# Performance work log

Hardware: AMD Instinct MI355X
Metric: run time of the kernel (lower is better)

The kernel has to match this reference:

```python
import jax, jax.numpy as jnp
import numpy as np
import math

V, D, H, L, T, B = 50257, 1024, 16, 8, 1024, 4
HD = D // H
EPS = 1e-5


def setup_inputs() -> dict:
    key = jax.random.key(0)
    ks = jax.random.split(key, 8)
    s = 0.02
    inp = {
        'context': jax.random.randint(ks[0], (B, T), 0, V, dtype=jnp.int32),
        'targets': jax.random.randint(ks[1], (B, T), 0, V, dtype=jnp.int32),
        'wte': jax.random.normal(ks[2], (V, D), jnp.float32) * s,  # tied with lm_head
        'wpe': jax.random.normal(ks[3], (T, D), jnp.float32) * s,
        'ln1_g': jnp.ones((L, D), jnp.float32), 'ln1_b': jnp.zeros((L, D), jnp.float32),
        'w_attn': jax.random.normal(ks[4], (L, 3 * D, D), jnp.float32) * s,
        'w_proj': jax.random.normal(ks[5], (L, D, D), jnp.float32) * s,
        'ln2_g': jnp.ones((L, D), jnp.float32), 'ln2_b': jnp.zeros((L, D), jnp.float32),
        'w_fc': jax.random.normal(ks[6], (L, 4 * D, D), jnp.float32) * s,
        'w_out': jax.random.normal(ks[7], (L, D, 4 * D), jnp.float32) * s,
        'lnf_g': jnp.ones((D,), jnp.float32), 'lnf_b': jnp.zeros((D,), jnp.float32),
    }
    return inp


def layer_norm(x, g, b):
    mu = jnp.mean(x, axis=-1, keepdims=True)
    var = jnp.var(x, axis=-1, keepdims=True)
    return (x - mu) * jax.lax.rsqrt(var + EPS) * g + b


def attention(x, w_attn, w_proj):
    # x: [B,T,D]; w_attn: [3D,D] (torch Linear convention: y = x @ W^T)
    qkv = x @ w_attn.T  # [B,T,3D]
    q, k, v = jnp.split(qkv, 3, axis=-1)
    q = q.reshape(B, T, H, HD).transpose(0, 2, 1, 3)  # [B,H,T,hd]
    k = k.reshape(B, T, H, HD).transpose(0, 2, 1, 3)
    v = v.reshape(B, T, H, HD).transpose(0, 2, 1, 3)
    att = jnp.einsum('bhtd,bhsd->bhts', q, k) * (1.0 / math.sqrt(HD))
    causal = jnp.tril(jnp.ones((T, T), dtype=bool))
    att = jnp.where(causal, att, -jnp.inf)
    att = jax.nn.softmax(att, axis=-1)
    y = jnp.einsum('bhts,bhsd->bhtd', att, v)
    y = y.transpose(0, 2, 1, 3).reshape(B, T, D)
    return y @ w_proj.T


def mlp(x, w_fc, w_out):
    h = jax.nn.gelu(x @ w_fc.T, approximate=False)  # exact GELU = torch nn.GELU()
    return h @ w_out.T


def reference(context, targets, wte, wpe, ln1_g, ln1_b, w_attn, w_proj,
              ln2_g, ln2_b, w_fc, w_out, lnf_g, lnf_b):
    x = wte[context] + wpe[jnp.arange(T)]  # [B,T,D]
    for i in range(L):
        x = x + attention(layer_norm(x, ln1_g[i], ln1_b[i]), w_attn[i], w_proj[i])
        x = x + mlp(layer_norm(x, ln2_g[i], ln2_b[i]), w_fc[i], w_out[i])
    x = layer_norm(x, lnf_g, lnf_b)
    logits = x @ wte.T  # tied lm_head, [B,T,V]
    # cross entropy with ignore_index=-1
    logp = jax.nn.log_softmax(logits, axis=-1)
    tgt = targets.reshape(-1)
    valid = tgt != -1
    safe_tgt = jnp.where(valid, tgt, 0)
    nll = -jnp.take_along_axis(logp.reshape(-1, V), safe_tgt[:, None], axis=-1)[:, 0]
    loss = jnp.sum(jnp.where(valid, nll, 0.0)) / jnp.maximum(jnp.sum(valid), 1)
    return logits, loss
```

## Files before the change

kernel.cpp:

```cpp
#include <hip/hip_runtime.h>
#include <cstdint>

#define V_SIZE 50257
#define V_PAD  50432
#define D_DIM  1024
#define H_NUM  16
#define L_NUM  8
#define T_LEN  1024
#define B_NUM  4
#define HD_DIM 64
#define M_ROWS 4096
#define LN_EPS 1e-5f

typedef __attribute__((ext_vector_type(8))) __bf16 bf16x8;
typedef __attribute__((ext_vector_type(4))) float f32x4;
typedef __attribute__((ext_vector_type(8))) unsigned short u16x8;

__device__ __forceinline__ unsigned short f2bf(float f) {
  unsigned u = __builtin_bit_cast(unsigned, f);
  u += 0x7fffu + ((u >> 16) & 1u);
  return (unsigned short)(u >> 16);
}

__device__ __forceinline__ void gload_lds16(const void* g, void* l) {
  typedef const __attribute__((address_space(1))) unsigned int* gp_t;
  typedef __attribute__((address_space(3))) unsigned int* lp_t;
  __builtin_amdgcn_global_load_lds((gp_t)g, (lp_t)l, 16, 0, 0);
}

#define BARSB() { __builtin_amdgcn_s_barrier(); __builtin_amdgcn_sched_barrier(0); }
#define LGKM0() { asm volatile("s_waitcnt lgkmcnt(0)" ::: "memory"); __builtin_amdgcn_sched_barrier(0); }

__global__ __launch_bounds__(256) void embed_kernel(const int* __restrict__ ctx,
                                                    const float* __restrict__ wte,
                                                    const float* __restrict__ wpe,
                                                    float* __restrict__ x) {
  int i = blockIdx.x * blockDim.x + threadIdx.x;
  if (i >= M_ROWS * D_DIM) return;
  int bt = i / D_DIM, d = i - bt * D_DIM;
  int t = bt & (T_LEN - 1);
  x[i] = wte[(size_t)ctx[bt] * D_DIM + d] + wpe[(size_t)t * D_DIM + d];
}

__global__ __launch_bounds__(256) void conv_layer_kernel(const float* __restrict__ wa,
                                                         const float* __restrict__ wp,
                                                         const float* __restrict__ wf,
                                                         const float* __restrict__ wo,
                                                         unsigned short* __restrict__ oa,
                                                         unsigned short* __restrict__ op,
                                                         unsigned short* __restrict__ of,
                                                         unsigned short* __restrict__ oo) {
  long i = (long)(blockIdx.x * 256 + threadIdx.x) * 8;
  const float* src; unsigned short* dst; long off;
  if (i < 3145728L)      { src = wa; dst = oa; off = i; }
  else if (i < 4194304L) { src = wp; dst = op; off = i - 3145728L; }
  else if (i < 8388608L) { src = wf; dst = of; off = i - 4194304L; }
  else                   { src = wo; dst = oo; off = i - 8388608L; }
  float4 v0 = *(const float4*)(src + off);
  float4 v1 = *(const float4*)(src + off + 4);
  u16x8 o;
  o[0] = f2bf(v0.x); o[1] = f2bf(v0.y); o[2] = f2bf(v0.z); o[3] = f2bf(v0.w);
  o[4] = f2bf(v1.x); o[5] = f2bf(v1.y); o[6] = f2bf(v1.z); o[7] = f2bf(v1.w);
  *(u16x8*)(dst + off) = o;
}

__global__ __launch_bounds__(256) void conv_kernel(const float* __restrict__ in,
                                                   unsigned short* __restrict__ out, long n) {
  long i = (long)(blockIdx.x * 256 + threadIdx.x) * 8;
  if (i >= n) return;
  float4 v0 = *(const float4*)(in + i);
  float4 v1 = *(const float4*)(in + i + 4);
  u16x8 o;
  o[0] = f2bf(v0.x); o[1] = f2bf(v0.y); o[2] = f2bf(v0.z); o[3] = f2bf(v0.w);
  o[4] = f2bf(v1.x); o[5] = f2bf(v1.y); o[6] = f2bf(v1.z); o[7] = f2bf(v1.w);
  *(u16x8*)(out + i) = o;
}

__global__ __launch_bounds__(256) void layernorm_kernel(const float* __restrict__ x,
                                                        const float* __restrict__ g,
                                                        const float* __restrict__ b,
                                                        unsigned short* __restrict__ o) {
  int r = blockIdx.x;
  int tid = threadIdx.x;
  const float* row = x + (size_t)r * D_DIM;
  float4 v = *(const float4*)(row + tid * 4);
  float s  = v.x + v.y + v.z + v.w;
  float s2 = v.x * v.x + v.y * v.y + v.z * v.z + v.w * v.w;
  #pragma unroll
  for (int off = 32; off; off >>= 1) {
    s  += __shfl_xor(s, off);
    s2 += __shfl_xor(s2, off);
  }
  __shared__ float a1[4], a2[4];
  int w = tid >> 6, lane = tid & 63;
  if (lane == 0) { a1[w] = s; a2[w] = s2; }
  __syncthreads();
  s  = a1[0] + a1[1] + a1[2] + a1[3];
  s2 = a2[0] + a2[1] + a2[2] + a2[3];
  float mu  = s * (1.0f / D_DIM);
  float var = s2 * (1.0f / D_DIM) - mu * mu;
  float rs  = rsqrtf(var + LN_EPS);
  int d = tid * 4;
  float4 gv = *(const float4*)(g + d);
  float4 bv = *(const float4*)(b + d);
  ushort4 ov;
  ov.x = f2bf((v.x - mu) * rs * gv.x + bv.x);
  ov.y = f2bf((v.y - mu) * rs * gv.y + bv.y);
  ov.z = f2bf((v.z - mu) * rs * gv.z + bv.z);
  ov.w = f2bf((v.w - mu) * rs * gv.w + bv.w);
  *(ushort4*)(o + (size_t)r * D_DIM + d) = ov;
}

template<int EPI>
__global__ __launch_bounds__(256) void mfma_gemm(const unsigned short* __restrict__ A,
                                                 const unsigned short* __restrict__ W,
                                                 const float* R, void* Cout,
                                                 int K, int ldc, int nreal) {
  __shared__ unsigned short As[128 * 32];
  __shared__ unsigned short Bs[128 * 32];
  const int tid  = threadIdx.x;
  const int wave = tid >> 6, lane = tid & 63;
  const int wr = wave >> 1, wc = wave & 1;
  const long row0 = (long)blockIdx.y * 128;
  const long col0 = (long)blockIdx.x * 128;
  f32x4 acc[4][4] = {};
  const int frow = lane & 15;
  const int fk   = (lane >> 4) * 8;
  const int b0 = wave * 2048 + lane * 16;
  for (int k0 = 0; k0 < K; k0 += 32) {
    #pragma unroll
    for (int c = 0; c < 2; ++c) {
      int b = b0 + c * 1024;
      int r = b >> 6, ke = (b & 63) >> 1;
      gload_lds16(A + (row0 + r) * (long)K + k0 + ke, (char*)As + b);
      gload_lds16(W + (col0 + r) * (long)K + k0 + ke, (char*)Bs + b);
    }
    __syncthreads();
    bf16x8 af[4], bfr[4];
    #pragma unroll
    for (int i = 0; i < 4; ++i)
      af[i] = *(const bf16x8*)(As + (wr * 64 + i * 16 + frow) * 32 + fk);
    #pragma unroll
    for (int j = 0; j < 4; ++j)
      bfr[j] = *(const bf16x8*)(Bs + (wc * 64 + j * 16 + frow) * 32 + fk);
    #pragma unroll
    for (int i = 0; i < 4; ++i)
      #pragma unroll
      for (int j = 0; j < 4; ++j)
        acc[i][j] = __builtin_amdgcn_mfma_f32_16x16x32_bf16(af[i], bfr[j], acc[i][j], 0, 0, 0);
    __syncthreads();
  }
  const int crow = (lane >> 4) * 4;
  const int ccol = lane & 15;
  #pragma unroll
  for (int i = 0; i < 4; ++i) {
    #pragma unroll
    for (int r = 0; r < 4; ++r) {
      long row = row0 + wr * 64 + i * 16 + crow + r;
      #pragma unroll
      for (int j = 0; j < 4; ++j) {
        long col = col0 + wc * 64 + j * 16 + ccol;
        float v = acc[i][j][r];
        if (EPI == 1) {
          ((float*)Cout)[row * (long)ldc + col] = v + R[row * (long)ldc + col];
        } else {
          ((float*)Cout)[row * (long)ldc + col] = v;
        }
      }
    }
  }
}

__device__ __forceinline__ void stage_chunk8(const unsigned short* __restrict__ base,
                                             long rbase, int K, long gk,
                                             char* cb, int tid) {
  #pragma unroll
  for (int j = 0; j < 2; ++j) {
    int db = j * 8192 + tid * 16;
    int lb = db ^ (((db >> 7) & 3) << 4);
    long r = lb >> 6;
    int e = (lb & 63) >> 1;
    gload_lds16(base + (rbase + r) * (long)K + gk + e, cb + db);
  }
}

__device__ __forceinline__ bf16x8 rdfrag(const char* cb, int rr, int lhi) {
  int p = (rr << 6) + (lhi << 4);
  p ^= ((rr >> 1) & 3) << 4;
  return *(const bf16x8*)(cb + p);
}

template<int EPI>
__global__ __launch_bounds__(512, 1) void gemm8p(const unsigned short* __restrict__ A,
                                                 const unsigned short* __restrict__ W,
                                                 void* Cout, int K, int ldc, int nreal,
                                                 int nbx, int xcd) {
  __shared__ char lds[131072];
  const int tid  = threadIdx.x;
  const int lane = tid & 63;
  const int wave = tid >> 6;
  const int wr = wave >> 2, wc = wave & 3;
  const int lhi = lane >> 4, llo = lane & 15;
  int bid = blockIdx.x;
  if (xcd) { int per = (int)gridDim.x >> 3; bid = (bid & 7) * per + (bid >> 3); }
  const int brow = bid % nbx;
  const int bcol = bid / nbx;
  const long row0 = (long)brow * 256;
  const long col0 = (long)bcol * 256;
  char* Ab0 = (char*)lds;
  char* Bb0 = (char*)lds + 65536;
  const int nt = K >> 6;

  stage_chunk8(A, row0, K, 0,  Ab0,         tid);
  stage_chunk8(W, col0, K, 0,  Bb0,         tid);
  stage_chunk8(A, row0, K, 32, Ab0 + 16384, tid);
  stage_chunk8(W, col0, K, 32, Bb0 + 16384, tid);
  if (nt > 1) {
    stage_chunk8(A, row0, K, 64, Ab0 + 32768, tid);
    stage_chunk8(W, col0, K, 64, Bb0 + 32768, tid);
    asm volatile("s_waitcnt vmcnt(4)" ::: "memory");
  } else {
    asm volatile("s_waitcnt vmcnt(0)" ::: "memory");
  }
  BARSB();

  f32x4 acc[8][4] = {};
  bf16x8 bb[4];
  for (int t = 0; t < nt; ++t) {
    char* Ac = Ab0 + (t & 1) * 32768;
    char* Bc = Bb0 + (t & 1) * 32768;
    char* An = Ab0 + ((t + 1) & 1) * 32768;
    char* Bn = Bb0 + ((t + 1) & 1) * 32768;
    bf16x8 aa[4];
    #pragma unroll
    for (int m = 0; m < 4; ++m) aa[m] = rdfrag(Ac, wr * 128 + m * 16 + llo, lhi);
    #pragma unroll
    for (int n = 0; n < 4; ++n) bb[n] = rdfrag(Bc, wc * 64 + n * 16 + llo, lhi);
    if (t + 1 < nt) stage_chunk8(A, row0, K, (long)(t + 1) * 64 + 32, An + 16384, tid);
    BARSB(); LGKM0();
    __builtin_amdgcn_s_setprio(1);
    #pragma unroll
    for (int m = 0; m < 4; ++m)
      #pragma unroll
      for (int n = 0; n < 4; ++n)
        acc[m][n] = __builtin_amdgcn_mfma_f32_16x16x32_bf16(aa[m], bb[n], acc[m][n], 0, 0, 0);
    __builtin_amdgcn_s_setprio(0);
    BARSB();
    #pragma unroll
    for (int m = 0; m < 4; ++m) aa[m] = rdfrag(Ac, wr * 128 + 64 + m * 16 + llo, lhi);
    if (t + 1 < nt) stage_chunk8(W, col0, K, (long)(t + 1) * 64 + 32, Bn + 16384, tid);
    BARSB(); LGKM0();
    __builtin_amdgcn_s_setprio(1);
    #pragma unroll
    for (int m = 0; m < 4; ++m)
      #pragma unroll
      for (int n = 0; n < 4; ++n)
        acc[m + 4][n] = __builtin_amdgcn_mfma_f32_16x16x32_bf16(aa[m], bb[n], acc[m + 4][n], 0, 0, 0);
    __builtin_amdgcn_s_setprio(0);
    BARSB();
    #pragma unroll
    for (int m = 0; m < 4; ++m) aa[m] = rdfrag(Ac + 16384, wr * 128 + m * 16 + llo, lhi);
    #pragma unroll
    for (int n = 0; n < 4; ++n) bb[n] = rdfrag(Bc + 16384, wc * 64 + n * 16 + llo, lhi);
    if (t + 2 < nt) stage_chunk8(A, row0, K, (long)(t + 2) * 64, Ac, tid);
    BARSB(); LGKM0();
    __builtin_amdgcn_s_setprio(1);
    #pragma unroll
    for (int m = 0; m < 4; ++m)
      #pragma unroll
      for (int n = 0; n < 4; ++n)
        acc[m][n] = __builtin_amdgcn_mfma_f32_16x16x32_bf16(aa[m], bb[n], acc[m][n], 0, 0, 0);
    __builtin_amdgcn_s_setprio(0);
    BARSB();
    #pragma unroll
    for (int m = 0; m < 4; ++m) aa[m] = rdfrag(Ac + 16384, wr * 128 + 64 + m * 16 + llo, lhi);
    if (t + 2 < nt) stage_chunk8(W, col0, K, (long)(t + 2) * 64, Bc, tid);
    BARSB(); LGKM0();
    __builtin_amdgcn_s_setprio(1);
    #pragma unroll
    for (int m = 0; m < 4; ++m)
      #pragma unroll
      for (int n = 0; n < 4; ++n)
        acc[m + 4][n] = __builtin_amdgcn_mfma_f32_16x16x32_bf16(aa[m], bb[n], acc[m + 4][n], 0, 0, 0);
    __builtin_amdgcn_s_setprio(0);
    if (t < nt - 2) {
      asm volatile("s_waitcnt vmcnt(4)" ::: "memory");
    } else {
      asm volatile("s_waitcnt vmcnt(0)" ::: "memory");
    }
    BARSB();
  }

  #pragma unroll
  for (int mi = 0; mi < 8; ++mi) {
    #pragma unroll
    for (int rg = 0; rg < 4; ++rg) {
      long row = row0 + wr * 128 + mi * 16 + lhi * 4 + rg;
      #pragma unroll
      for (int n = 0; n < 4; ++n) {
        long col = col0 + wc * 64 + n * 16 + llo;
        float v = acc[mi][n][rg];
        if (EPI == 0) {
          if (col < nreal) ((float*)Cout)[row * (long)ldc + col] = v;
        } else if (EPI == 2) {
          float gl = 0.5f * v * (1.0f + erff(v * 0.70710678118654752440f));
          ((unsigned short*)Cout)[row * (long)ldc + col] = f2bf(gl);
        } else {
          ((unsigned short*)Cout)[row * (long)ldc + col] = f2bf(v);
        }
      }
    }
  }
}

__global__ __launch_bounds__(256) void flash_attn_kernel(const unsigned short* __restrict__ qkv,
                                                         unsigned short* __restrict__ y) {
  __shared__ unsigned short Kls[64 * 64];
  __shared__ unsigned short Vtls[64 * 64];
  __shared__ unsigned short Pls[4][16 * 64];
  const int tid = threadIdx.x, wave = tid >> 6, lane = tid & 63;
  const int qt = blockIdx.x;
  const int h = blockIdx.y & (H_NUM - 1), b = blockIdx.y >> 4;
  const int q0 = qt * 64;
  const int lhi = lane >> 4, llo = lane & 15;

  const int qrow = q0 + wave * 16 + llo;
  const unsigned short* qptr =
      qkv + ((size_t)(b * T_LEN + qrow)) * 3072 + h * HD_DIM + lhi * 8;
  const bf16x8 qa0 = *(const bf16x8*)qptr;
  const bf16x8 qa1 = *(const bf16x8*)(qptr + 32);

  f32x4 o[4] = {};
  float m[4] = {-1e30f, -1e30f, -1e30f, -1e30f};
  float l[4] = {0.f, 0.f, 0.f, 0.f};

  const unsigned short* kg = qkv + (size_t)b * T_LEN * 3072 + D_DIM + h * HD_DIM;
  const unsigned short* vg = kg + D_DIM;

  const int krow = tid >> 2, kcol = (tid & 3) * 16;
  const int vs0 = (tid >> 3) * 2, vd0 = (tid & 7) * 8;

  const int ntiles = qt + 1;
  for (int st = 0; st < ntiles; ++st) {
    const int s0 = st * 64;
    {
      const unsigned short* src = kg + (size_t)(s0 + krow) * 3072 + kcol;
      u16x8 a = *(const u16x8*)src;
      u16x8 c = *(const u16x8*)(src + 8);
      int base = krow * 128 + kcol * 2;
      int sw = (krow & 7) << 4;
      *(u16x8*)((char*)Kls + ((base) ^ sw))      = a;
      *(u16x8*)((char*)Kls + ((base + 16) ^ sw)) = c;
    }
    {
      const unsigned short* src = vg + (size_t)(s0 + vs0) * 3072 + vd0;
      u16x8 a = *(const u16x8*)src;
      u16x8 c = *(const u16x8*)(src + 3072);
      #pragma unroll
      for (int j = 0; j < 8; ++j) {
        int d = vd0 + j;
        unsigned val = (unsigned)a[j] | ((unsigned)c[j] << 16);
        *(unsigned*)((char*)Vtls + ((d * 128 + vs0 * 2) ^ ((d & 7) << 4))) = val;
      }
    }
    __syncthreads();

    f32x4 s_acc[4] = {};
    #pragma unroll
    for (int kt = 0; kt < 4; ++kt) {
      int kr = kt * 16 + llo;
      int sw = (kr & 7) << 4;
      bf16x8 kb0 = *(const bf16x8*)((char*)Kls + ((kr * 128 + lhi * 16) ^ sw));
      bf16x8 kb1 = *(const bf16x8*)((char*)Kls + ((kr * 128 + 64 + lhi * 16) ^ sw));
      s_acc[kt] = __builtin_amdgcn_mfma_f32_16x16x32_bf16(qa0, kb0, s_acc[kt], 0, 0, 0);
      s_acc[kt] = __builtin_amdgcn_mfma_f32_16x16x32_bf16(qa1, kb1, s_acc[kt], 0, 0, 0);
    }

    float p[4][4];
    float tmax[4] = {-1e30f, -1e30f, -1e30f, -1e30f};
    const int qg = q0 + wave * 16 + lhi * 4;
    #pragma unroll
    for (int kt = 0; kt < 4; ++kt) {
      int ks = s0 + kt * 16 + llo;
      #pragma unroll
      for (int r = 0; r < 4; ++r) {
        float sv = (ks <= qg + r) ? s_acc[kt][r] * 0.125f : -1e30f;
        p[kt][r] = sv;
        tmax[r] = fmaxf(tmax[r], sv);
      }
    }
    #pragma unroll
    for (int r = 0; r < 4; ++r) {
      #pragma unroll
      for (int off = 1; off < 16; off <<= 1)
        tmax[r] = fmaxf(tmax[r], __shfl_xor(tmax[r], off));
      float mn = fmaxf(m[r], tmax[r]);
      float corr = __expf(m[r] - mn);
      m[r] = mn;
      float ps = 0.f;
      #pragma unroll
      for (int kt = 0; kt < 4; ++kt) {
        p[kt][r] = __expf(p[kt][r] - mn);
        ps += p[kt][r];
      }
      #pragma unroll
      for (int off = 1; off < 16; off <<= 1)
        ps += __shfl_xor(ps, off);
      l[r] = l[r] * corr + ps;
      #pragma unroll
      for (int dt = 0; dt < 4; ++dt) o[dt][r] *= corr;
    }

    unsigned short* pw = Pls[wave];
    #pragma unroll
    for (int r = 0; r < 4; ++r) {
      int q = lhi * 4 + r;
      int sw = (q & 7) << 4;
      #pragma unroll
      for (int kt = 0; kt < 4; ++kt) {
        int k = kt * 16 + llo;
        *(unsigned short*)((char*)pw + ((q * 128 + k * 2) ^ sw)) = f2bf(p[kt][r]);
      }
    }
    asm volatile("s_waitcnt lgkmcnt(0)" ::: "memory");

    int psw = (llo & 7) << 4;
    bf16x8 pa0 = *(const bf16x8*)((char*)pw + ((llo * 128 + lhi * 16) ^ psw));
    bf16x8 pa1 = *(const bf16x8*)((char*)pw + ((llo * 128 + 64 + lhi * 16) ^ psw));
    #pragma unroll
    for (int dt = 0; dt < 4; ++dt) {
      int vr = dt * 16 + llo;
      int sw = (vr & 7) << 4;
      bf16x8 vb0 = *(const bf16x8*)((char*)Vtls + ((vr * 128 + lhi * 16) ^ sw));
      bf16x8 vb1 = *(const bf16x8*)((char*)Vtls + ((vr * 128 + 64 + lhi * 16) ^ sw));
      o[dt] = __builtin_amdgcn_mfma_f32_16x16x32_bf16(pa0, vb0, o[dt], 0, 0, 0);
      o[dt] = __builtin_amdgcn_mfma_f32_16x16x32_bf16(pa1, vb1, o[dt], 0, 0, 0);
    }
    __syncthreads();
  }

  #pragma unroll
  for (int r = 0; r < 4; ++r) {
    long row = q0 + wave * 16 + lhi * 4 + r;
    float inv = 1.0f / l[r];
    #pragma unroll
    for (int dt = 0; dt < 4; ++dt) {
      long col = h * HD_DIM + dt * 16 + llo;
      y[(row + (size_t)b * T_LEN) * D_DIM + col] = f2bf(o[dt][r] * inv);
    }
  }
}

__global__ __launch_bounds__(256) void loss_rows_kernel(const float* __restrict__ logits,
                                                        const int* __restrict__ tgt,
                                                        float* __restrict__ nll,
                                                        float* __restrict__ vld) {
  int r = blockIdx.x;
  int tid = threadIdx.x;
  const float* row = logits + (size_t)r * V_SIZE;
  float mx = -1e30f;
  for (int i = tid; i < V_SIZE; i += 256) mx = fmaxf(mx, row[i]);
  #pragma unroll
  for (int off = 32; off; off >>= 1) mx = fmaxf(mx, __shfl_xor(mx, off));
  __shared__ float sm[4], ss[4];
  int w = tid >> 6, lane = tid & 63;
  if (lane == 0) sm[w] = mx;
  __syncthreads();
  mx = fmaxf(fmaxf(sm[0], sm[1]), fmaxf(sm[2], sm[3]));
  float se = 0.f;
  for (int i = tid; i < V_SIZE; i += 256) se += expf(row[i] - mx);
  #pragma unroll
  for (int off = 32; off; off >>= 1) se += __shfl_xor(se, off);
  if (lane == 0) ss[w] = se;
  __syncthreads();
  if (tid == 0) {
    se = ss[0] + ss[1] + ss[2] + ss[3];
    int tg = tgt[r];
    if (tg != -1) { nll[r] = mx + logf(se) - row[tg]; vld[r] = 1.0f; }
    else          { nll[r] = 0.f;                     vld[r] = 0.f; }
  }
}

__global__ __launch_bounds__(256) void loss_reduce_kernel(const float* __restrict__ nll,
                                                          const float* __restrict__ vld,
                                                          float* __restrict__ out) {
  int tid = threadIdx.x;
  float s = 0.f, c = 0.f;
  for (int i = tid; i < M_ROWS; i += 256) { s += nll[i]; c += vld[i]; }
  #pragma unroll
  for (int off = 32; off; off >>= 1) { s += __shfl_xor(s, off); c += __shfl_xor(c, off); }
  __shared__ float s1[4], s2[4];
  int w = tid >> 6, lane = tid & 63;
  if (lane == 0) { s1[w] = s; s2[w] = c; }
  __syncthreads();
  if (tid == 0) {
    s = s1[0] + s1[1] + s1[2] + s1[3];
    c = s2[0] + s2[1] + s2[2] + s2[3];
    out[0] = s / fmaxf(c, 1.0f);
  }
}

extern "C" void kernel_launch(void* const* d_in, const int* in_sizes, int n_in,
                              void* d_out, int out_size, void* d_ws, size_t ws_size,
                              hipStream_t stream) {
  const int*   ctx    = (const int*)d_in[0];
  const int*   tgt    = (const int*)d_in[1];
  const float* wte    = (const float*)d_in[2];
  const float* wpe    = (const float*)d_in[3];
  const float* ln1_g  = (const float*)d_in[4];
  const float* ln1_b  = (const float*)d_in[5];
  const float* w_attn = (const float*)d_in[6];
  const float* w_proj = (const float*)d_in[7];
  const float* ln2_g  = (const float*)d_in[8];
  const float* ln2_b  = (const float*)d_in[9];
  const float* w_fc   = (const float*)d_in[10];
  const float* w_out  = (const float*)d_in[11];
  const float* lnf_g  = (const float*)d_in[12];
  const float* lnf_b  = (const float*)d_in[13];

  float* outp   = (float*)d_out;
  float* logits = outp;
  float* loss   = outp + (size_t)M_ROWS * V_SIZE;

  char* ws = (char*)d_ws;
  float*          x      = (float*)(ws + 0);
  unsigned short* xn     = (unsigned short*)(ws + 16777216);
  unsigned short* qkv    = (unsigned short*)(ws + 25165824);
  unsigned short* y      = (unsigned short*)(ws + 50331648);
  unsigned short* h      = (unsigned short*)(ws + 58720256);
  unsigned short* wa_bf  = (unsigned short*)(ws + 92274688);
  unsigned short* wp_bf  = (unsigned short*)(ws + 98566144);
  unsigned short* wf_bf  = (unsigned short*)(ws + 100663296);
  unsigned short* wo_bf  = (unsigned short*)(ws + 109051904);
  unsigned short* wte_bf = (unsigned short*)(ws + 25165824);
  float*          nll    = (float*)(ws + 128450560);
  float*          vld    = (float*)(ws + 128466944);

  embed_kernel<<<(M_ROWS * D_DIM + 255) / 256, 256, 0, stream>>>(ctx, wte, wpe, x);

  for (int l = 0; l < L_NUM; ++l) {
    conv_layer_kernel<<<6144, 256, 0, stream>>>(
        w_attn + (size_t)l * 3 * D_DIM * D_DIM, w_proj + (size_t)l * D_DIM * D_DIM,
        w_fc + (size_t)l * 4 * D_DIM * D_DIM, w_out + (size_t)l * D_DIM * 4 * D_DIM,
        wa_bf, wp_bf, wf_bf, wo_bf);
    layernorm_kernel<<<M_ROWS, 256, 0, stream>>>(x, ln1_g + l * D_DIM, ln1_b + l * D_DIM, xn);
    gemm8p<3><<<12 * 16, 512, 0, stream>>>(
        xn, wa_bf, qkv, D_DIM, 3 * D_DIM, 3 * D_DIM, 16, 0);
    flash_attn_kernel<<<dim3(T_LEN / 64, B_NUM * H_NUM), 256, 0, stream>>>(qkv, y);
    mfma_gemm<1><<<dim3(D_DIM / 128, M_ROWS / 128), 256, 0, stream>>>(
        y, wp_bf, x, x, D_DIM, D_DIM, D_DIM);
    layernorm_kernel<<<M_ROWS, 256, 0, stream>>>(x, ln2_g + l * D_DIM, ln2_b + l * D_DIM, xn);
    gemm8p<2><<<16 * 16, 512, 0, stream>>>(
        xn, wf_bf, h, D_DIM, 4 * D_DIM, 4 * D_DIM, 16, 0);
    mfma_gemm<1><<<dim3(D_DIM / 128, M_ROWS / 128), 256, 0, stream>>>(
        h, wo_bf, x, x, 4 * D_DIM, D_DIM, D_DIM);
  }

  layernorm_kernel<<<M_ROWS, 256, 0, stream>>>(x, lnf_g, lnf_b, xn);
  conv_kernel<<<25129, 256, 0, stream>>>(wte, wte_bf, (long)V_SIZE * D_DIM);
  hipMemsetAsync(wte_bf + (size_t)V_SIZE * D_DIM, 0,
                 (size_t)(V_PAD - V_SIZE) * D_DIM * sizeof(unsigned short), stream);
  gemm8p<0><<<197 * 16, 512, 0, stream>>>(
      xn, wte_bf, logits, D_DIM, V_SIZE, V_SIZE, 16, 1);
  loss_rows_kernel<<<M_ROWS, 256, 0, stream>>>(logits, tgt, nll, vld);
  loss_reduce_kernel<<<1, 256, 0, stream>>>(nll, vld, loss);
}
```

Before: 3.656 ms.

## Deepen GEMM B-tile prefetch, use online softmax in loss, enable XCD remap

The gemm8p main loop now issues W-tile loads one half-step earlier, so three stages are in flight at the prologue, and uses finer vmcnt waits to hide global latency. The loss-row kernel replaces its two passes over each logits row (max, then sum of exp) with a single online-softmax pass, halving reads of the large logits buffer. The QKV and FC GEMM launches also turn on XCD-aware block remapping to improve L2 locality. The risks are hazards from the reordered LDS buffer reuse and the fast __expf approximation in the loss.

Measured after the change: 3.490 ms. 4.5% less time.

```diff
diff --git a/kernel.cpp b/kernel.cpp
--- a/kernel.cpp
+++ b/kernel.cpp
@@ -216,9 +216,10 @@
   stage_chunk8(A, row0, K, 32, Ab0 + 16384, tid);
   stage_chunk8(W, col0, K, 32, Bb0 + 16384, tid);
   if (nt > 1) {
+    stage_chunk8(W, col0, K, 64, Bb0 + 32768, tid);
     stage_chunk8(A, row0, K, 64, Ab0 + 32768, tid);
-    stage_chunk8(W, col0, K, 64, Bb0 + 32768, tid);
-    asm volatile("s_waitcnt vmcnt(4)" ::: "memory");
+    stage_chunk8(W, col0, K, 96, Bb0 + 49152, tid);
+    asm volatile("s_waitcnt vmcnt(10)" ::: "memory");
   } else {
     asm volatile("s_waitcnt vmcnt(0)" ::: "memory");
   }
@@ -230,7 +231,6 @@
     char* Ac = Ab0 + (t & 1) * 32768;
     char* Bc = Bb0 + (t & 1) * 32768;
     char* An = Ab0 + ((t + 1) & 1) * 32768;
-    char* Bn = Bb0 + ((t + 1) & 1) * 32768;
     bf16x8 aa[4];
     #pragma unroll
     for (int m = 0; m < 4; ++m) aa[m] = rdfrag(Ac, wr * 128 + m * 16 + llo, lhi);
@@ -248,7 +248,7 @@
     BARSB();
     #pragma unroll
     for (int m = 0; m < 4; ++m) aa[m] = rdfrag(Ac, wr * 128 + 64 + m * 16 + llo, lhi);
-    if (t + 1 < nt) stage_chunk8(W, col0, K, (long)(t + 1) * 64 + 32, Bn + 16384, tid);
+    if (t + 2 < nt) stage_chunk8(W, col0, K, (long)(t + 2) * 64, Bc, tid);
     BARSB(); LGKM0();
     __builtin_amdgcn_s_setprio(1);
     #pragma unroll
@@ -257,6 +257,9 @@
       for (int n = 0; n < 4; ++n)
         acc[m + 4][n] = __builtin_amdgcn_mfma_f32_16x16x32_bf16(aa[m], bb[n], acc[m + 4][n], 0, 0, 0);
     __builtin_amdgcn_s_setprio(0);
+    if (t <= nt - 3)      { asm volatile("s_waitcnt vmcnt(10)" ::: "memory"); }
+    else if (t == nt - 2) { asm volatile("s_waitcnt vmcnt(8)"  ::: "memory"); }
+    else                  { asm volatile("s_waitcnt vmcnt(0)"  ::: "memory"); }
     BARSB();
     #pragma unroll
     for (int m = 0; m < 4; ++m) aa[m] = rdfrag(Ac + 16384, wr * 128 + m * 16 + llo, lhi);
@@ -274,7 +277,7 @@
     BARSB();
     #pragma unroll
     for (int m = 0; m < 4; ++m) aa[m] = rdfrag(Ac + 16384, wr * 128 + 64 + m * 16 + llo, lhi);
-    if (t + 2 < nt) stage_chunk8(W, col0, K, (long)(t + 2) * 64, Bc, tid);
+    if (t + 2 < nt) stage_chunk8(W, col0, K, (long)(t + 2) * 64 + 32, Bc + 16384, tid);
     BARSB(); LGKM0();
     __builtin_amdgcn_s_setprio(1);
     #pragma unroll
@@ -283,11 +286,9 @@
       for (int n = 0; n < 4; ++n)
         acc[m + 4][n] = __builtin_amdgcn_mfma_f32_16x16x32_bf16(aa[m], bb[n], acc[m + 4][n], 0, 0, 0);
     __builtin_amdgcn_s_setprio(0);
-    if (t < nt - 2) {
-      asm volatile("s_waitcnt vmcnt(4)" ::: "memory");
-    } else {
-      asm volatile("s_waitcnt vmcnt(0)" ::: "memory");
-    }
+    if (t <= nt - 3)      { asm volatile("s_waitcnt vmcnt(10)" ::: "memory"); }
+    else if (t == nt - 2) { asm volatile("s_waitcnt vmcnt(4)"  ::: "memory"); }
+    else                  { asm volatile("s_waitcnt vmcnt(0)"  ::: "memory"); }
     BARSB();
   }
 
@@ -458,25 +459,35 @@
   int r = blockIdx.x;
   int tid = threadIdx.x;
   const float* row = logits + (size_t)r * V_SIZE;
-  float mx = -1e30f;
-  for (int i = tid; i < V_SIZE; i += 256) mx = fmaxf(mx, row[i]);
-  #pragma unroll
-  for (int off = 32; off; off >>= 1) mx = fmaxf(mx, __shfl_xor(mx, off));
+  float lm = -1e30f, ls = 0.f;
+  for (int i = tid; i < V_SIZE; i += 256) {
+    float v = row[i];
+    float nm = fmaxf(lm, v);
+    ls = ls * __expf(lm - nm) + __expf(v - nm);
+    lm = nm;
+  }
+  #pragma unroll
+  for (int off = 1; off < 64; off <<= 1) {
+    float om = __shfl_xor(lm, off);
+    float os = __shfl_xor(ls, off);
+    float nm = fmaxf(lm, om);
+    ls = ls * __expf(lm - nm) + os * __expf(om - nm);
+    lm = nm;
+  }
   __shared__ float sm[4], ss[4];
   int w = tid >> 6, lane = tid & 63;
-  if (lane == 0) sm[w] = mx;
-  __syncthreads();
-  mx = fmaxf(fmaxf(sm[0], sm[1]), fmaxf(sm[2], sm[3]));
-  float se = 0.f;
-  for (int i = tid; i < V_SIZE; i += 256) se += expf(row[i] - mx);
-  #pragma unroll
-  for (int off = 32; off; off >>= 1) se += __shfl_xor(se, off);
-  if (lane == 0) ss[w] = se;
+  if (lane == 0) { sm[w] = lm; ss[w] = ls; }
   __syncthreads();
   if (tid == 0) {
-    se = ss[0] + ss[1] + ss[2] + ss[3];
+    lm = sm[0]; ls = ss[0];
+    #pragma unroll
+    for (int i = 1; i < 4; ++i) {
+      float nm = fmaxf(lm, sm[i]);
+      ls = ls * __expf(lm - nm) + ss[i] * __expf(sm[i] - nm);
+      lm = nm;
+    }
     int tg = tgt[r];
-    if (tg != -1) { nll[r] = mx + logf(se) - row[tg]; vld[r] = 1.0f; }
+    if (tg != -1) { nll[r] = lm + logf(ls) - row[tg]; vld[r] = 1.0f; }
     else          { nll[r] = 0.f;                     vld[r] = 0.f; }
   }
 }
@@ -545,13 +556,13 @@
         wa_bf, wp_bf, wf_bf, wo_bf);
     layernorm_kernel<<<M_ROWS, 256, 0, stream>>>(x, ln1_g + l * D_DIM, ln1_b + l * D_DIM, xn);
     gemm8p<3><<<12 * 16, 512, 0, stream>>>(
-        xn, wa_bf, qkv, D_DIM, 3 * D_DIM, 3 * D_DIM, 16, 0);
+        xn, wa_bf, qkv, D_DIM, 3 * D_DIM, 3 * D_DIM, 16, 1);
     flash_attn_kernel<<<dim3(T_LEN / 64, B_NUM * H_NUM), 256, 0, stream>>>(qkv, y);
     mfma_gemm<1><<<dim3(D_DIM / 128, M_ROWS / 128), 256, 0, stream>>>(
         y, wp_bf, x, x, D_DIM, D_DIM, D_DIM);
     layernorm_kernel<<<M_ROWS, 256, 0, stream>>>(x, ln2_g + l * D_DIM, ln2_b + l * D_DIM, xn);
     gemm8p<2><<<16 * 16, 512, 0, stream>>>(
-        xn, wf_bf, h, D_DIM, 4 * D_DIM, 4 * D_DIM, 16, 0);
+        xn, wf_bf, h, D_DIM, 4 * D_DIM, 4 * D_DIM, 16, 1);
     mfma_gemm<1><<<dim3(D_DIM / 128, M_ROWS / 128), 256, 0, stream>>>(
         h, wo_bf, x, x, 4 * D_DIM, D_DIM, D_DIM);
   }
```
